# Kernel optimization log

Hardware: AMD Instinct MI355X
Metric: run time of the kernel (lower is better)

The kernel has to match this reference:

```python
import jax, jax.numpy as jnp
import numpy as np

B = 16384        # batch of states
D_IN = 512       # num_inputs (= num_gating_input)
H0 = 1024        # hidden_layer[0]
H1 = 1024        # hidden_layer[1]
D_OUT = 64       # num_outputs
E = 8            # num_experts (hard-coded in module)
G_H = 128        # gate MLP hidden width


def setup_inputs() -> dict:
    key = jax.random.key(0)
    ks = jax.random.split(key, 14)
    s = 0.05
    return {
        "inputs": jax.random.normal(ks[0], (B, D_IN), dtype=jnp.float32),
        # gate MLP: Linear(D_IN,128) -> relu -> Linear(128,128) -> relu -> Linear(128,E)
        "gw1": jax.random.normal(ks[1], (D_IN, G_H), dtype=jnp.float32) * s,
        "gb1": jnp.zeros((G_H,), dtype=jnp.float32),
        "gw2": jax.random.normal(ks[2], (G_H, G_H), dtype=jnp.float32) * s,
        "gb2": jnp.zeros((G_H,), dtype=jnp.float32),
        "gw3": jax.random.normal(ks[3], (G_H, E), dtype=jnp.float32) * s,
        "gb3": jnp.zeros((E,), dtype=jnp.float32),
        # expert (policy) layers: (weight [E,in,out], bias [E,1,out])
        "w0": jax.random.normal(ks[4], (E, D_IN, H0), dtype=jnp.float32) * s,
        "b0": jax.random.normal(ks[5], (E, 1, H0), dtype=jnp.float32) * s,
        "w1": jax.random.normal(ks[6], (E, H0, H1), dtype=jnp.float32) * s,
        "b1": jax.random.normal(ks[7], (E, 1, H1), dtype=jnp.float32) * s,
        "w2": jax.random.normal(ks[8], (E, H1, D_OUT), dtype=jnp.float32) * s,
        "b2": jax.random.normal(ks[9], (E, 1, D_OUT), dtype=jnp.float32) * s,
    }


def reference(inputs, gw1, gb1, gw2, gb2, gw3, gb3, w0, b0, w1, b1, w2, b2):
    # Gate: softmax over experts, torch code reshapes to [E, B, 1] via .t().unsqueeze(-1);
    # here keep g as [B, E] and contract the expert axis directly.
    h = jax.nn.relu(inputs @ gw1 + gb1)
    h = jax.nn.relu(h @ gw2 + gb2)
    g = jax.nn.softmax(h @ gw3 + gb3, axis=1)  # [B, E]

    def expert_layer(x, w, b, act):
        # out.matmul(weight) : [B,d] x [E,d,h] -> [E,B,h]; +bias; *gate; sum over E
        y = jnp.einsum('bd,edh->ebh', x, w) + b      # [E, B, h]
        return act(jnp.einsum('be,ebh->bh', g, y))   # [B, h]

    x = expert_layer(inputs, w0, b0, jax.nn.relu)
    x = expert_layer(x, w1, b1, jax.nn.relu)
    x = expert_layer(x, w2, b2, jnp.tanh)
    return x
```

## Files before the change

kernel.cpp:

```cpp
#include <hip/hip_runtime.h>
#include <hip/hip_bf16.h>
#include <cstdint>

#define DI __device__ __forceinline__

typedef unsigned short ushort_t;
using u16x8  = __attribute__((ext_vector_type(8))) unsigned short;
using bf16x8 = __attribute__((ext_vector_type(8))) __bf16;
using f32x4  = __attribute__((ext_vector_type(4))) float;

typedef const __attribute__((address_space(1))) void GVOID;
typedef __attribute__((address_space(3))) void LVOID;

enum { BB = 16384, DIN = 512, H0 = 1024, H1 = 1024, DOUT = 64, NE = 8, GH = 128 };

DI void async_ld16(const void* g, void* l) {
    __builtin_amdgcn_global_load_lds((GVOID*)g, (LVOID*)l, 16, 0, 0);
}

DI unsigned short f2bf(float f) {
    union { float f; unsigned u; } v; v.f = f;
    unsigned r = v.u + 0x7FFF + ((v.u >> 16) & 1);
    return (unsigned short)(r >> 16);
}
DI float bf2f(unsigned short u) { return __uint_as_float(((unsigned)u) << 16); }
DI f32x4 zero4() { f32x4 v = {0.f, 0.f, 0.f, 0.f}; return v; }

#define BARRIER() do { __builtin_amdgcn_s_barrier(); asm volatile("" ::: "memory"); } while (0)
#define LGKM0()   asm volatile("s_waitcnt lgkmcnt(0)" ::: "memory")

__global__ void f32_to_bf16_vec(const float* __restrict__ in, ushort_t* __restrict__ out) {
    const int i = (blockIdx.x * 256 + threadIdx.x) * 8;
    const float4 a = *(const float4*)&in[i];
    const float4 b = *(const float4*)&in[i + 4];
    u16x8 o;
    o[0] = f2bf(a.x); o[1] = f2bf(a.y); o[2] = f2bf(a.z); o[3] = f2bf(a.w);
    o[4] = f2bf(b.x); o[5] = f2bf(b.y); o[6] = f2bf(b.z); o[7] = f2bf(b.w);
    *(u16x8*)&out[i] = o;
}

__global__ void transpose_convert(const float* __restrict__ W, ushort_t* __restrict__ Wt,
                                  int K, int N, int Kext) {
    __shared__ float t[64][69];
    const int tid = threadIdx.x;
    const int k0 = blockIdx.x * 64, n0 = blockIdx.y * 64;
    for (int rr = tid >> 4; rr < 64; rr += 16) {
        const int c = (tid & 15) * 4;
        const float4 v = *(const float4*)&W[(size_t)(k0 + rr) * N + n0 + c];
        t[rr][c] = v.x; t[rr][c + 1] = v.y; t[rr][c + 2] = v.z; t[rr][c + 3] = v.w;
    }
    __syncthreads();
    for (int nn = tid >> 3; nn < 64; nn += 32) {
        const int k8 = (tid & 7) * 8;
        u16x8 o;
#pragma unroll
        for (int j = 0; j < 8; ++j) o[j] = f2bf(t[k8 + j][nn]);
        *(u16x8*)&Wt[(size_t)(n0 + nn) * Kext + k0 + k8] = o;
    }
}

__global__ void bias_fill(const float* __restrict__ bias, ushort_t* __restrict__ Wt,
                          int N, int K, int Kext) {
    const int n = blockIdx.x, c = threadIdx.x;
    Wt[(size_t)n * Kext + K + c] = (c < 8) ? f2bf(bias[(size_t)c * N + n]) : (ushort_t)0;
}

__global__ void gate3_softmax(const ushort_t* __restrict__ h2, const float* __restrict__ gw3,
                              const float* __restrict__ gb3, float* __restrict__ g,
                              ushort_t* __restrict__ Gx) {
    __shared__ float w[GH * NE];
    const int tid = threadIdx.x;
    for (int i = tid; i < GH * NE; i += 256) w[i] = gw3[i];
    __syncthreads();
    const int b = blockIdx.x * 256 + tid;
    float lg[NE];
#pragma unroll
    for (int e = 0; e < NE; ++e) lg[e] = gb3[e];
    const ushort_t* row = h2 + (size_t)b * GH;
    for (int h8 = 0; h8 < GH; h8 += 8) {
        const u16x8 v = *(const u16x8*)&row[h8];
#pragma unroll
        for (int j = 0; j < 8; ++j) {
            const float xv = bf2f(v[j]);
#pragma unroll
            for (int e = 0; e < NE; ++e) lg[e] += xv * w[(h8 + j) * NE + e];
        }
    }
    float mx = lg[0];
#pragma unroll
    for (int e = 1; e < NE; ++e) mx = fmaxf(mx, lg[e]);
    float s = 0.f;
#pragma unroll
    for (int e = 0; e < NE; ++e) { lg[e] = __expf(lg[e] - mx); s += lg[e]; }
    const float inv = 1.f / s;
#pragma unroll
    for (int e = 0; e < NE; ++e) g[(size_t)b * NE + e] = lg[e] * inv;
    ushort_t* gxr = Gx + (size_t)b * 64;
    u16x8 o;
#pragma unroll
    for (int e = 0; e < NE; ++e) o[e] = f2bf(lg[e] * inv);
    *(u16x8*)gxr = o;
    u16x8 z = {0, 0, 0, 0, 0, 0, 0, 0};
#pragma unroll
    for (int i = 1; i < 8; ++i) *(u16x8*)(gxr + i * 8) = z;
}

template <int TPE64, int STRIDEX>
__global__ __launch_bounds__(512, 2) void gemm256p(
    const ushort_t* __restrict__ X,
    const ushort_t* __restrict__ Gx,
    const ushort_t* __restrict__ Wt,
    const float* __restrict__ gvec,
    ushort_t* __restrict__ out,
    int N, int Kext) {
    constexpr int TE64 = NE * TPE64;
    const int NT = Kext >> 6;
    const int tid = threadIdx.x;
    const int wid = tid >> 6, l = tid & 63;
    const int wm = wid >> 2, wn = wid & 3;
    const int lr = l & 15, lk = l >> 4;

    const int b = blockIdx.x;
    const int xcd = b & 7, j2 = b >> 3;
    const int by = j2 & 3, bx = xcd + 8 * (j2 >> 2);
    const int bm0 = bx * 256, bn0 = by * 256;

    __shared__ __align__(1024) char lA[2][2][16384];
    __shared__ __align__(1024) char lB[2][2][16384];
    __shared__ float rtab[256 * 8];

    for (int r = tid; r < 256; r += 512) {
        const float* gr = gvec + (size_t)(bm0 + r) * 8;
        float ge[8];
#pragma unroll
        for (int e = 0; e < 8; ++e) ge[e] = gr[e];
#pragma unroll
        for (int e = 0; e < 7; ++e) rtab[r * 8 + e] = ge[e] / ge[e + 1];
        rtab[r * 8 + 7] = ge[7];
    }

    const int srow = (wid << 3) + (l >> 3);
    const int scol = (((l & 7) ^ (srow & 7)) << 3);
    auto stA = [&](int t, int h) {
        char* dst = (char*)lA[t & 1][h] + (wid << 10);
        if (t < TE64) {
            const ushort_t* s = X + (size_t)(bm0 + h * 128 + srow) * STRIDEX
                                  + (t & (TPE64 - 1)) * 64 + scol;
            async_ld16(s, dst);
            async_ld16(s + (size_t)64 * STRIDEX, dst + 8192);
        } else {
            const ushort_t* s = Gx + (size_t)(bm0 + h * 128 + srow) * 64 + scol;
            async_ld16(s, dst);
            async_ld16(s + 64 * 64, dst + 8192);
        }
    };
    auto stB = [&](int t, int h) {
        char* dst = (char*)lB[t & 1][h] + (wid << 10);
        const ushort_t* s = Wt + (size_t)(bn0 + h * 128 + srow) * (size_t)Kext
                              + t * 64 + scol;
        async_ld16(s, dst);
        async_ld16(s + (size_t)64 * Kext, dst + 8192);
    };

    const int chunk0 = ((lk ^ (lr & 7)) << 4);
    const int aoff = lr * 128;
    const int boff = ((wn & 1) << 13) + lr * 128;

    f32x4 acc[8][4];
#pragma unroll
    for (int m = 0; m < 8; ++m)
#pragma unroll
        for (int n = 0; n < 4; ++n) acc[m][n] = zero4();

    stB(0, 0); stB(0, 1); stA(0, 0); stA(0, 1);
    stB(1, 0); stB(1, 1);
    LGKM0();
    asm volatile("s_waitcnt vmcnt(4)" ::: "memory");
    BARRIER();

    for (int t = 0; t < NT; ++t) {
        const char* Ah = (const char*)lA[t & 1][wm] + aoff;
        const char* Bh = (const char*)lB[t & 1][wn >> 1] + boff;
        bf16x8 a0[4], a1[4], b0[4], b1[4];

#pragma unroll
        for (int m = 0; m < 4; ++m) {
            a0[m] = *(const bf16x8*)(Ah + m * 2048 + chunk0);
            a1[m] = *(const bf16x8*)(Ah + m * 2048 + (chunk0 ^ 64));
        }
#pragma unroll
        for (int n = 0; n < 4; ++n) {
            b0[n] = *(const bf16x8*)(Bh + n * 2048 + chunk0);
            b1[n] = *(const bf16x8*)(Bh + n * 2048 + (chunk0 ^ 64));
        }
        if (t + 1 < NT) { stA(t + 1, 0); stA(t + 1, 1); }
        BARRIER();
        __builtin_amdgcn_s_setprio(1);
#pragma unroll
        for (int m = 0; m < 4; ++m)
#pragma unroll
            for (int n = 0; n < 4; ++n) {
                acc[m][n] = __builtin_amdgcn_mfma_f32_16x16x32_bf16(a0[m], b0[n], acc[m][n], 0, 0, 0);
                acc[m][n] = __builtin_amdgcn_mfma_f32_16x16x32_bf16(a1[m], b1[n], acc[m][n], 0, 0, 0);
            }
        __builtin_amdgcn_s_setprio(0);
        BARRIER();

#pragma unroll
        for (int m = 0; m < 4; ++m) {
            a0[m] = *(const bf16x8*)(Ah + (m + 4) * 2048 + chunk0);
            a1[m] = *(const bf16x8*)(Ah + (m + 4) * 2048 + (chunk0 ^ 64));
        }
        if (t + 2 < NT) { stB(t + 2, 0); stB(t + 2, 1); }
        BARRIER();
        __builtin_amdgcn_s_setprio(1);
#pragma unroll
        for (int m = 0; m < 4; ++m)
#pragma unroll
            for (int n = 0; n < 4; ++n) {
                acc[m + 4][n] = __builtin_amdgcn_mfma_f32_16x16x32_bf16(a0[m], b0[n], acc[m + 4][n], 0, 0, 0);
                acc[m + 4][n] = __builtin_amdgcn_mfma_f32_16x16x32_bf16(a1[m], b1[n], acc[m + 4][n], 0, 0, 0);
            }
        __builtin_amdgcn_s_setprio(0);

        if (t < TE64 && ((t + 1) & (TPE64 - 1)) == 0) {
            const int e = t / TPE64;
#pragma unroll
            for (int m = 0; m < 8; ++m)
#pragma unroll
                for (int q = 0; q < 4; ++q) {
                    const float r = rtab[(wm * 128 + m * 16 + lk * 4 + q) * 8 + e];
#pragma unroll
                    for (int n = 0; n < 4; ++n) acc[m][n][q] *= r;
                }
        }
        if (t + 2 < NT) {
            asm volatile("s_waitcnt vmcnt(4)" ::: "memory");
            BARRIER();
        } else if (t + 1 < NT) {
            asm volatile("s_waitcnt vmcnt(0)" ::: "memory");
            BARRIER();
        }
    }

#pragma unroll
    for (int m = 0; m < 8; ++m) {
        const int row = bm0 + wm * 128 + m * 16 + lk * 4;
#pragma unroll
        for (int n = 0; n < 4; ++n) {
            const int col = bn0 + wn * 64 + n * 16 + lr;
#pragma unroll
            for (int q = 0; q < 4; ++q) {
                const float v = fmaxf(acc[m][n][q], 0.f);
                out[(size_t)(row + q) * N + col] = f2bf(v);
            }
        }
    }
}

template <int BN, int TPE, int ACT, bool GATED, bool OUTF32>
__global__ __launch_bounds__(256, 2) void moe_gemm(
    const ushort_t* __restrict__ X, const ushort_t* __restrict__ Wt,
    const float* __restrict__ gvec, const float* __restrict__ bias,
    void* __restrict__ outv, int M, int N, int K, int Klen) {
    constexpr int BM = 128, BK = 64;
    constexpr int NF = BN / 32;
    const int tid = threadIdx.x;
    const int wid = tid >> 6, lane = tid & 63;
    const int lr = lane & 15, lk = lane >> 4;
    const int bm0 = blockIdx.x * BM;
    const int bn0 = blockIdx.y * BN;
    const int wm0 = (wid >> 1) * 64;
    const int wn0 = (wid & 1) * (BN / 2);
    const int koff = blockIdx.z * Klen;
    const int te0 = (TPE > 0) ? koff / (TPE * BK) : 0;

    __shared__ short lds_a[BM * BK];
    __shared__ short lds_b[BN * BK];
    __shared__ float lds_g[BM * 8];
    __shared__ float lds_bias[8 * BN];

    if constexpr (GATED) {
        ((f32x4*)lds_g)[tid] = ((const f32x4*)(gvec + (size_t)bm0 * 8))[tid];
        if constexpr (ACT != 2) {
            for (int i = tid; i < 8 * BN; i += 256) {
                const int e = i / BN, n = i - e * BN;
                lds_bias[i] = bias[(size_t)e * N + bn0 + n];
            }
        }
    }

    f32x4 acc_t[4][NF], acc_p[4][NF];
#pragma unroll
    for (int m = 0; m < 4; ++m)
#pragma unroll
        for (int n = 0; n < NF; ++n) { acc_t[m][n] = zero4(); acc_p[m][n] = zero4(); }

    f32x4(&amain)[4][NF] = GATED ? acc_p : acc_t;

    const int xstride = (TPE > 0) ? TPE * BK : K;
    const int NT = Klen / BK;
    for (int kt = 0; kt < NT; ++kt) {
        int kcolA;
        if constexpr (TPE > 0) kcolA = (kt % TPE) * BK; else kcolA = kt * BK;
        {
            const ushort_t* abase = X + (size_t)bm0 * xstride + kcolA;
#pragma unroll
            for (int c = wid; c < (BM * BK * 2) / 1024; c += 4) {
                const int off = c * 1024 + lane * 16;
                const int r = off >> 7, cbyte = off & 127;
                async_ld16((const char*)abase + (size_t)r * (xstride * 2) + cbyte,
                           (char*)lds_a + c * 1024);
            }
            const ushort_t* bbase = Wt + (size_t)bn0 * K + koff + kt * BK;
#pragma unroll
            for (int c = wid; c < (BN * BK * 2) / 1024; c += 4) {
                const int off = c * 1024 + lane * 16;
                const int r = off >> 7, cbyte = off & 127;
                async_ld16((const char*)bbase + (size_t)r * ((size_t)K * 2) + cbyte,
                           (char*)lds_b + c * 1024);
            }
        }
        __syncthreads();

        bf16x8 af[2][4], bfr[2][NF];
#pragma unroll
        for (int k2 = 0; k2 < 2; ++k2) {
#pragma unroll
            for (int m = 0; m < 4; ++m)
                af[k2][m] = *(const bf16x8*)&lds_a[(wm0 + m * 16 + lr) * BK + k2 * 32 + lk * 8];
#pragma unroll
            for (int n = 0; n < NF; ++n)
                bfr[k2][n] = *(const bf16x8*)&lds_b[(wn0 + n * 16 + lr) * BK + k2 * 32 + lk * 8];
        }
#pragma unroll
        for (int m = 0; m < 4; ++m)
#pragma unroll
            for (int n = 0; n < NF; ++n) {
                amain[m][n] = __builtin_amdgcn_mfma_f32_16x16x32_bf16(af[0][m], bfr[0][n], amain[m][n], 0, 0, 0);
                amain[m][n] = __builtin_amdgcn_mfma_f32_16x16x32_bf16(af[1][m], bfr[1][n], amain[m][n], 0, 0, 0);
            }

        if constexpr (TPE > 0 && GATED) {
            if ((kt + 1) % TPE == 0) {
                const int e = te0 + kt / TPE;
#pragma unroll
                for (int m = 0; m < 4; ++m)
#pragma unroll
                    for (int q = 0; q < 4; ++q) {
                        const float gw = lds_g[(wm0 + m * 16 + lk * 4 + q) * 8 + e];
#pragma unroll
                        for (int n = 0; n < NF; ++n) {
                            acc_t[m][n][q] += gw * acc_p[m][n][q];
                            acc_p[m][n][q] = 0.f;
                        }
                    }
            }
        }
        __syncthreads();
    }

#pragma unroll
    for (int m = 0; m < 4; ++m)
#pragma unroll
        for (int n = 0; n < NF; ++n)
#pragma unroll
            for (int q = 0; q < 4; ++q) {
                const int row = wm0 + m * 16 + lk * 4 + q;
                const int col = wn0 + n * 16 + lr;
                float v = acc_t[m][n][q];
                if constexpr (ACT != 2) {
                    if constexpr (GATED) {
                        float bs = 0.f;
#pragma unroll
                        for (int e = 0; e < 8; ++e) bs += lds_g[row * 8 + e] * lds_bias[e * BN + col];
                        v += bs;
                    } else {
                        v += bias[bn0 + col];
                    }
                }
                if constexpr (ACT == 0) v = fmaxf(v, 0.f);
                else if constexpr (ACT == 1) v = tanhf(v);
                const size_t oidx = (size_t)blockIdx.z * M * N + (size_t)(bm0 + row) * N + (bn0 + col);
                if constexpr (OUTF32) ((float*)outv)[oidx] = v;
                else ((ushort_t*)outv)[oidx] = f2bf(v);
            }
}

__global__ void splitk_reduce8(const float* __restrict__ part, const float* __restrict__ g,
                               const float* __restrict__ b2, float* __restrict__ out) {
    __shared__ float bs[8 * 64];
    const int tid = threadIdx.x;
    for (int i = tid; i < 512; i += 256) bs[i] = b2[i];
    __syncthreads();
    const int idx = blockIdx.x * 256 + tid;
    const int bb = idx >> 6, n = idx & 63;
    const float* gr = g + (size_t)bb * 8;
    float v = 0.f;
#pragma unroll
    for (int e = 0; e < 8; ++e)
        v += gr[e] * (part[(size_t)e * BB * 64 + idx] + bs[e * 64 + n]);
    out[idx] = tanhf(v);
}

extern "C" void kernel_launch(void* const* d_in, const int* in_sizes, int n_in,
                              void* d_out, int out_size, void* d_ws, size_t ws_size,
                              hipStream_t stream) {
    const float* inputs = (const float*)d_in[0];
    const float* gw1 = (const float*)d_in[1];
    const float* gb1 = (const float*)d_in[2];
    const float* gw2 = (const float*)d_in[3];
    const float* gb2 = (const float*)d_in[4];
    const float* gw3 = (const float*)d_in[5];
    const float* gb3 = (const float*)d_in[6];
    const float* w0 = (const float*)d_in[7];
    const float* b0 = (const float*)d_in[8];
    const float* w1 = (const float*)d_in[9];
    const float* b1 = (const float*)d_in[10];
    const float* w2 = (const float*)d_in[11];
    const float* b2 = (const float*)d_in[12];
    (void)in_sizes; (void)n_in; (void)out_size; (void)ws_size;

    constexpr int KE0 = NE * DIN + 64;
    constexpr int KE1 = NE * H0 + 64;

    char* ws = (char*)d_ws;
    ushort_t* x0b = (ushort_t*)(ws + 0);
    ushort_t* W0t = (ushort_t*)(ws + 16777216);
    ushort_t* G1t = (ushort_t*)(ws + 25427968);
    ushort_t* G2t = (ushort_t*)(ws + 25559040);
    ushort_t* h1b = (ushort_t*)(ws + 25591808);
    ushort_t* h2b = (ushort_t*)(ws + 29786112);
    ushort_t* x2b = (ushort_t*)(ws + 0);
    ushort_t* W1t = (ushort_t*)(ws + 33980416);
    ushort_t* W2t = (ushort_t*)(ws + 51019776);
    float*    gv  = (float*)(ws + 52068352);
    ushort_t* Gx  = (ushort_t*)(ws + 52592640);
    ushort_t* x1b = (ushort_t*)(ws + 56786944);
    float*    p2  = (float*)(ws + 56786944);

    f32_to_bf16_vec<<<dim3((BB * DIN) / (256 * 8)), 256, 0, stream>>>(inputs, x0b);
    transpose_convert<<<dim3((NE * DIN) / 64, H0 / 64), 256, 0, stream>>>(w0, W0t, NE * DIN, H0, KE0);
    transpose_convert<<<dim3((NE * H0) / 64, H1 / 64), 256, 0, stream>>>(w1, W1t, NE * H0, H1, KE1);
    transpose_convert<<<dim3((NE * H1) / 64, DOUT / 64), 256, 0, stream>>>(w2, W2t, NE * H1, DOUT, NE * H1);
    transpose_convert<<<dim3(DIN / 64, GH / 64), 256, 0, stream>>>(gw1, G1t, DIN, GH, DIN);
    transpose_convert<<<dim3(GH / 64, GH / 64), 256, 0, stream>>>(gw2, G2t, GH, GH, GH);
    bias_fill<<<dim3(H0), 64, 0, stream>>>(b0, W0t, H0, NE * DIN, KE0);
    bias_fill<<<dim3(H1), 64, 0, stream>>>(b1, W1t, H1, NE * H0, KE1);

    moe_gemm<64, 0, 0, false, false><<<dim3(BB / 128, GH / 64), 256, 0, stream>>>(
        x0b, G1t, nullptr, gb1, h1b, BB, GH, DIN, DIN);
    moe_gemm<64, 0, 0, false, false><<<dim3(BB / 128, GH / 64), 256, 0, stream>>>(
        h1b, G2t, nullptr, gb2, h2b, BB, GH, GH, GH);
    gate3_softmax<<<dim3(BB / 256), 256, 0, stream>>>(h2b, gw3, gb3, gv, Gx);

    gemm256p<DIN / 64, DIN><<<dim3((BB / 256) * (H0 / 256)), 512, 0, stream>>>(
        x0b, Gx, W0t, gv, x1b, H0, KE0);
    gemm256p<H0 / 64, H0><<<dim3((BB / 256) * (H1 / 256)), 512, 0, stream>>>(
        x1b, Gx, W1t, gv, x2b, H1, KE1);

    moe_gemm<64, 16, 2, false, true><<<dim3(BB / 128, DOUT / 64, 8), 256, 0, stream>>>(
        x2b, W2t, nullptr, nullptr, p2, BB, DOUT, NE * H1, H1);
    splitk_reduce8<<<dim3((BB * DOUT) / 256), 256, 0, stream>>>(p2, gv, b2, (float*)d_out);
}
```

Before: 432.4 us.

## Replace 256x256 BK64 expert GEMM with 256x128 BK32 tiles at higher occupancy

```diff
diff --git a/kernel.cpp b/kernel.cpp
--- a/kernel.cpp
+++ b/kernel.cpp
@@ -95,38 +95,36 @@
     const float inv = 1.f / s;
 #pragma unroll
     for (int e = 0; e < NE; ++e) g[(size_t)b * NE + e] = lg[e] * inv;
-    ushort_t* gxr = Gx + (size_t)b * 64;
+    ushort_t* gxr = Gx + (size_t)b * 32;
     u16x8 o;
 #pragma unroll
     for (int e = 0; e < NE; ++e) o[e] = f2bf(lg[e] * inv);
     *(u16x8*)gxr = o;
     u16x8 z = {0, 0, 0, 0, 0, 0, 0, 0};
 #pragma unroll
-    for (int i = 1; i < 8; ++i) *(u16x8*)(gxr + i * 8) = z;
-}
-
-template <int TPE64, int STRIDEX>
-__global__ __launch_bounds__(512, 2) void gemm256p(
+    for (int i = 1; i < 4; ++i) *(u16x8*)(gxr + i * 8) = z;
+}
+
+template <int TPE32, int STRIDEX>
+__global__ __launch_bounds__(512, 4) void gemm2b(
     const ushort_t* __restrict__ X,
     const ushort_t* __restrict__ Gx,
     const ushort_t* __restrict__ Wt,
     const float* __restrict__ gvec,
     ushort_t* __restrict__ out,
     int N, int Kext) {
-    constexpr int TE64 = NE * TPE64;
-    const int NT = Kext >> 6;
+    constexpr int TE32 = NE * TPE32;
+    const int NT = Kext >> 5;
     const int tid = threadIdx.x;
     const int wid = tid >> 6, l = tid & 63;
-    const int wm = wid >> 2, wn = wid & 3;
+    const int wm = wid >> 1, wn = wid & 1;
     const int lr = l & 15, lk = l >> 4;
 
     const int b = blockIdx.x;
-    const int xcd = b & 7, j2 = b >> 3;
-    const int by = j2 & 3, bx = xcd + 8 * (j2 >> 2);
-    const int bm0 = bx * 256, bn0 = by * 256;
-
-    __shared__ __align__(1024) char lA[2][2][16384];
-    __shared__ __align__(1024) char lB[2][2][16384];
+    const int bn0 = (b & 7) * 128, bm0 = (b >> 3) * 256;
+
+    __shared__ __align__(1024) char lA[2][16384];
+    __shared__ __align__(1024) char lB[2][8192];
     __shared__ float rtab[256 * 8];
 
     for (int r = tid; r < 256; r += 512) {
@@ -139,103 +137,88 @@
         rtab[r * 8 + 7] = ge[7];
     }
 
-    const int srow = (wid << 3) + (l >> 3);
-    const int scol = (((l & 7) ^ (srow & 7)) << 3);
-    auto stA = [&](int t, int h) {
-        char* dst = (char*)lA[t & 1][h] + (wid << 10);
-        if (t < TE64) {
-            const ushort_t* s = X + (size_t)(bm0 + h * 128 + srow) * STRIDEX
-                                  + (t & (TPE64 - 1)) * 64 + scol;
+    const int sr = (wid << 4) + (l >> 2);
+    const int scol = (((l & 3) ^ ((l >> 2) & 3)) << 3);
+    auto stA = [&](int t) {
+        char* dst = (char*)lA[t & 1] + (wid << 10);
+        if (t < TE32) {
+            const ushort_t* s = X + (size_t)(bm0 + sr) * STRIDEX
+                                  + (t % TPE32) * 32 + scol;
             async_ld16(s, dst);
-            async_ld16(s + (size_t)64 * STRIDEX, dst + 8192);
+            async_ld16(s + (size_t)128 * STRIDEX, dst + 8192);
         } else {
-            const ushort_t* s = Gx + (size_t)(bm0 + h * 128 + srow) * 64 + scol;
+            const ushort_t* s = Gx + (size_t)(bm0 + sr) * 32 + scol;
             async_ld16(s, dst);
-            async_ld16(s + 64 * 64, dst + 8192);
+            async_ld16(s + 128 * 32, dst + 8192);
         }
     };
-    auto stB = [&](int t, int h) {
-        char* dst = (char*)lB[t & 1][h] + (wid << 10);
-        const ushort_t* s = Wt + (size_t)(bn0 + h * 128 + srow) * (size_t)Kext
-                              + t * 64 + scol;
+    auto stB = [&](int t) {
+        char* dst = (char*)lB[t & 1] + (wid << 10);
+        const ushort_t* s = Wt + (size_t)(bn0 + sr) * (size_t)Kext + t * 32 + scol;
         async_ld16(s, dst);
-        async_ld16(s + (size_t)64 * Kext, dst + 8192);
     };
 
-    const int chunk0 = ((lk ^ (lr & 7)) << 4);
-    const int aoff = lr * 128;
-    const int boff = ((wn & 1) << 13) + lr * 128;
-
-    f32x4 acc[8][4];
-#pragma unroll
-    for (int m = 0; m < 8; ++m)
+    const int chunk0 = ((lk ^ (lr & 3)) << 4);
+    const int aoff = (wm * 64 + lr) * 64 + chunk0;
+    const int boff = (wn * 64 + lr) * 64 + chunk0;
+
+    f32x4 acc[4][4];
+#pragma unroll
+    for (int m = 0; m < 4; ++m)
 #pragma unroll
         for (int n = 0; n < 4; ++n) acc[m][n] = zero4();
 
-    stB(0, 0); stB(0, 1); stA(0, 0); stA(0, 1);
-    stB(1, 0); stB(1, 1);
+    stA(0); stB(0);
+    stB(1);
     LGKM0();
-    asm volatile("s_waitcnt vmcnt(4)" ::: "memory");
+    asm volatile("s_waitcnt vmcnt(1)" ::: "memory");
     BARRIER();
 
     for (int t = 0; t < NT; ++t) {
-        const char* Ah = (const char*)lA[t & 1][wm] + aoff;
-        const char* Bh = (const char*)lB[t & 1][wn >> 1] + boff;
-        bf16x8 a0[4], a1[4], b0[4], b1[4];
-
-#pragma unroll
-        for (int m = 0; m < 4; ++m) {
-            a0[m] = *(const bf16x8*)(Ah + m * 2048 + chunk0);
-            a1[m] = *(const bf16x8*)(Ah + m * 2048 + (chunk0 ^ 64));
-        }
-#pragma unroll
-        for (int n = 0; n < 4; ++n) {
-            b0[n] = *(const bf16x8*)(Bh + n * 2048 + chunk0);
-            b1[n] = *(const bf16x8*)(Bh + n * 2048 + (chunk0 ^ 64));
-        }
-        if (t + 1 < NT) { stA(t + 1, 0); stA(t + 1, 1); }
+        const char* Ah = (const char*)lA[t & 1] + aoff;
+        const char* Bh = (const char*)lB[t & 1] + boff;
+        bf16x8 a0[2], b0[4];
+
+#pragma unroll
+        for (int n = 0; n < 4; ++n) b0[n] = *(const bf16x8*)(Bh + n * 1024);
+#pragma unroll
+        for (int m = 0; m < 2; ++m) a0[m] = *(const bf16x8*)(Ah + m * 1024);
+        if (t + 1 < NT) stA(t + 1);
         BARRIER();
         __builtin_amdgcn_s_setprio(1);
 #pragma unroll
-        for (int m = 0; m < 4; ++m)
-#pragma unroll
-            for (int n = 0; n < 4; ++n) {
+        for (int m = 0; m < 2; ++m)
+#pragma unroll
+            for (int n = 0; n < 4; ++n)
                 acc[m][n] = __builtin_amdgcn_mfma_f32_16x16x32_bf16(a0[m], b0[n], acc[m][n], 0, 0, 0);
-                acc[m][n] = __builtin_amdgcn_mfma_f32_16x16x32_bf16(a1[m], b1[n], acc[m][n], 0, 0, 0);
-            }
         __builtin_amdgcn_s_setprio(0);
         BARRIER();
 
 #pragma unroll
-        for (int m = 0; m < 4; ++m) {
-            a0[m] = *(const bf16x8*)(Ah + (m + 4) * 2048 + chunk0);
-            a1[m] = *(const bf16x8*)(Ah + (m + 4) * 2048 + (chunk0 ^ 64));
-        }
-        if (t + 2 < NT) { stB(t + 2, 0); stB(t + 2, 1); }
+        for (int m = 0; m < 2; ++m) a0[m] = *(const bf16x8*)(Ah + (m + 2) * 1024);
+        if (t + 2 < NT) stB(t + 2);
         BARRIER();
         __builtin_amdgcn_s_setprio(1);
 #pragma unroll
-        for (int m = 0; m < 4; ++m)
-#pragma unroll
-            for (int n = 0; n < 4; ++n) {
-                acc[m + 4][n] = __builtin_amdgcn_mfma_f32_16x16x32_bf16(a0[m], b0[n], acc[m + 4][n], 0, 0, 0);
-                acc[m + 4][n] = __builtin_amdgcn_mfma_f32_16x16x32_bf16(a1[m], b1[n], acc[m + 4][n], 0, 0, 0);
-            }
+        for (int m = 0; m < 2; ++m)
+#pragma unroll
+            for (int n = 0; n < 4; ++n)
+                acc[m + 2][n] = __builtin_amdgcn_mfma_f32_16x16x32_bf16(a0[m], b0[n], acc[m + 2][n], 0, 0, 0);
         __builtin_amdgcn_s_setprio(0);
 
-        if (t < TE64 && ((t + 1) & (TPE64 - 1)) == 0) {
-            const int e = t / TPE64;
-#pragma unroll
-            for (int m = 0; m < 8; ++m)
+        if (t < TE32 && ((t + 1) % TPE32) == 0) {
+            const int e = t / TPE32;
+#pragma unroll
+            for (int m = 0; m < 4; ++m)
 #pragma unroll
                 for (int q = 0; q < 4; ++q) {
-                    const float r = rtab[(wm * 128 + m * 16 + lk * 4 + q) * 8 + e];
+                    const float r = rtab[(wm * 64 + m * 16 + lk * 4 + q) * 8 + e];
 #pragma unroll
                     for (int n = 0; n < 4; ++n) acc[m][n][q] *= r;
                 }
         }
         if (t + 2 < NT) {
-            asm volatile("s_waitcnt vmcnt(4)" ::: "memory");
+            asm volatile("s_waitcnt vmcnt(1)" ::: "memory");
             BARRIER();
         } else if (t + 1 < NT) {
             asm volatile("s_waitcnt vmcnt(0)" ::: "memory");
@@ -244,8 +227,8 @@
     }
 
 #pragma unroll
-    for (int m = 0; m < 8; ++m) {
-        const int row = bm0 + wm * 128 + m * 16 + lk * 4;
+    for (int m = 0; m < 4; ++m) {
+        const int row = bm0 + wm * 64 + m * 16 + lk * 4;
 #pragma unroll
         for (int n = 0; n < 4; ++n) {
             const int col = bn0 + wn * 64 + n * 16 + lr;
@@ -421,8 +404,8 @@
     const float* b2 = (const float*)d_in[12];
     (void)in_sizes; (void)n_in; (void)out_size; (void)ws_size;
 
-    constexpr int KE0 = NE * DIN + 64;
-    constexpr int KE1 = NE * H0 + 64;
+    constexpr int KE0 = NE * DIN + 32;
+    constexpr int KE1 = NE * H0 + 32;
 
     char* ws = (char*)d_ws;
     ushort_t* x0b = (ushort_t*)(ws + 0);
@@ -445,8 +428,8 @@
     transpose_convert<<<dim3((NE * H1) / 64, DOUT / 64), 256, 0, stream>>>(w2, W2t, NE * H1, DOUT, NE * H1);
     transpose_convert<<<dim3(DIN / 64, GH / 64), 256, 0, stream>>>(gw1, G1t, DIN, GH, DIN);
     transpose_convert<<<dim3(GH / 64, GH / 64), 256, 0, stream>>>(gw2, G2t, GH, GH, GH);
-    bias_fill<<<dim3(H0), 64, 0, stream>>>(b0, W0t, H0, NE * DIN, KE0);
-    bias_fill<<<dim3(H1), 64, 0, stream>>>(b1, W1t, H1, NE * H0, KE1);
+    bias_fill<<<dim3(H0), 32, 0, stream>>>(b0, W0t, H0, NE * DIN, KE0);
+    bias_fill<<<dim3(H1), 32, 0, stream>>>(b1, W1t, H1, NE * H0, KE1);
 
     moe_gemm<64, 0, 0, false, false><<<dim3(BB / 128, GH / 64), 256, 0, stream>>>(
         x0b, G1t, nullptr, gb1, h1b, BB, GH, DIN, DIN);
@@ -454,9 +437,9 @@
         h1b, G2t, nullptr, gb2, h2b, BB, GH, GH, GH);
     gate3_softmax<<<dim3(BB / 256), 256, 0, stream>>>(h2b, gw3, gb3, gv, Gx);
 
-    gemm256p<DIN / 64, DIN><<<dim3((BB / 256) * (H0 / 256)), 512, 0, stream>>>(
+    gemm2b<DIN / 32, DIN><<<dim3((BB / 256) * (H0 / 128)), 512, 0, stream>>>(
         x0b, Gx, W0t, gv, x1b, H0, KE0);
-    gemm256p<H0 / 64, H0><<<dim3((BB / 256) * (H1 / 256)), 512, 0, stream>>>(
+    gemm2b<H0 / 32, H0><<<dim3((BB / 256) * (H1 / 128)), 512, 0, stream>>>(
         x1b, Gx, W1t, gv, x2b, H1, KE1);
 
     moe_gemm<64, 16, 2, false, true><<<dim3(BB / 128, DOUT / 64, 8), 256, 0, stream>>>(
```

Result: slower. 571.1 us (+32.1%).
